# Kernel optimization log

Hardware: AMD Instinct MI355X
Metric: run time of the kernel (lower is better)

## Reference

```python
import jax, jax.numpy as jnp
import numpy as np

DELTA = 1
DROP_DC = False
EPS = 1e-8


def _shell_labels(D, H, W, delta):
    # radial frequency magnitude in cycles/voxel, assuming cubic-ish volume
    fx = jnp.fft.fftfreq(D)[:, None, None]
    fy = jnp.fft.fftfreq(H)[None, :, None]
    fz = jnp.fft.fftfreq(W)[None, None, :]
    r = jnp.sqrt(fx * fx + fy * fy + fz * fz)  # [D,H,W]
    n = min(D, H, W)
    nbins = n // (2 * delta)          # shells up to Nyquist (0.5 cyc/voxel)
    df = delta / n                    # shell width in frequency units
    labels = jnp.minimum((r / df).astype(jnp.int32), nbins)  # overflow bin = nbins
    return labels.reshape(-1), nbins


def setup_inputs() -> dict:
    key = jax.random.key(0)
    k1, k2 = jax.random.split(key)
    shape = (2, 1, 256, 256, 256)
    img_ref = jax.random.normal(k1, shape, dtype=jnp.float32)
    img_pred = jax.random.normal(k2, shape, dtype=jnp.float32)
    return {"img_ref": img_ref, "img_pred": img_pred}


def reference(img_ref, img_pred):
    B, C, D, H, W = img_ref.shape
    labels, nbins = _shell_labels(D, H, W, DELTA)

    F1 = jnp.fft.fftn(img_ref, axes=(-3, -2, -1))   # complex64 [B,C,D,H,W]
    F2 = jnp.fft.fftn(img_pred, axes=(-3, -2, -1))

    cross = jnp.real(F1 * jnp.conj(F2)).reshape(B * C, -1)
    p1 = (jnp.real(F1) ** 2 + jnp.imag(F1) ** 2).reshape(B * C, -1)
    p2 = (jnp.real(F2) ** 2 + jnp.imag(F2) ** 2).reshape(B * C, -1)

    def seg(x):  # radial shell sum; drop the overflow bin beyond Nyquist
        return jax.ops.segment_sum(x, labels, num_segments=nbins + 1)[:nbins]

    num = jax.vmap(seg)(cross)   # [B*C, nbins]
    d1 = jax.vmap(seg)(p1)
    d2 = jax.vmap(seg)(p2)

    fsc = num / jnp.sqrt(d1 * d2 + EPS)
    if DROP_DC:
        fsc = fsc[:, 1:]
    loss = 1.0 - jnp.mean(fsc ** 2)
    return loss
```

## Files before the change

kernel.cpp:

```cpp
#include <hip/hip_runtime.h>
#include <math.h>

#define NDIM 256
#define VOL  (NDIM*NDIM*NDIM)
#define NB   128

__device__ __forceinline__ int dr4(int x) {
    int b = (int)(__brev((unsigned)x) >> 24);
    return ((b >> 1) & 0x55) | ((b << 1) & 0xAA);
}
__device__ __forceinline__ float2 cmul(float2 a, float2 b) {
    return make_float2(a.x * b.x - a.y * b.y, a.x * b.y + a.y * b.x);
}
__device__ __forceinline__ float2 cadd(float2 a, float2 b){ return make_float2(a.x+b.x, a.y+b.y); }
__device__ __forceinline__ float2 csub(float2 a, float2 b){ return make_float2(a.x-b.x, a.y-b.y); }
__device__ __forceinline__ float2 cmuli_neg(float2 a){ return make_float2(a.y, -a.x); }
__device__ __forceinline__ float2 cmuli_pos(float2 a){ return make_float2(-a.y, a.x); }

__global__ __launch_bounds__(256) void fftz_pack(const float* __restrict__ re_in,
                                                 const float* __restrict__ im_in,
                                                 float2* __restrict__ out)
{
    __shared__ float2 buf[4][2][NDIM];
    const int t = threadIdx.x;
    const int w = t >> 6, j = t & 63;
    const int L = blockIdx.x * 4 + w;
    const float* rp = re_in + (size_t)L * NDIM;
    const float* ip = im_in + (size_t)L * NDIM;

    float2 v0 = make_float2(rp[j      ], ip[j      ]);
    float2 v1 = make_float2(rp[j +  64], ip[j +  64]);
    float2 v2 = make_float2(rp[j + 128], ip[j + 128]);
    float2 v3 = make_float2(rp[j + 192], ip[j + 192]);

    {
        float2 t0=cadd(v0,v2), t1=csub(v0,v2), t2=cadd(v1,v3), t3=csub(v1,v3);
        buf[w][0][4*j    ] = cadd(t0, t2);
        buf[w][0][4*j + 1] = cadd(t1, cmuli_neg(t3));
        buf[w][0][4*j + 2] = csub(t0, t2);
        buf[w][0][4*j + 3] = cadd(t1, cmuli_pos(t3));
    }
    __builtin_amdgcn_sched_barrier(0);

    int p = 0;
    #pragma unroll
    for (int stage = 1; stage <= 2; ++stage) {
        const int Ns = (stage == 1) ? 4 : 16;
        const int jm = j & (Ns - 1);
        float2 a0 = buf[w][p][j      ];
        float2 a1 = buf[w][p][j +  64];
        float2 a2 = buf[w][p][j + 128];
        float2 a3 = buf[w][p][j + 192];
        float sn, cs;
        __sincosf(-(float)(2.0 * M_PI) * (float)jm / (float)(4 * Ns), &sn, &cs);
        float2 w1 = make_float2(cs, sn);
        float2 w2 = cmul(w1, w1);
        float2 w3 = cmul(w2, w1);
        a1 = cmul(a1, w1); a2 = cmul(a2, w2); a3 = cmul(a3, w3);
        float2 t0=cadd(a0,a2), t1=csub(a0,a2), t2=cadd(a1,a3), t3=csub(a1,a3);
        const int idxD = (j / Ns) * (4 * Ns) + jm;
        buf[w][p^1][idxD         ] = cadd(t0, t2);
        buf[w][p^1][idxD +     Ns] = cadd(t1, cmuli_neg(t3));
        buf[w][p^1][idxD + 2 * Ns] = csub(t0, t2);
        buf[w][p^1][idxD + 3 * Ns] = cadd(t1, cmuli_pos(t3));
        p ^= 1;
        __builtin_amdgcn_sched_barrier(0);
    }

    {
        float2 a0 = buf[w][p][j      ];
        float2 a1 = buf[w][p][j +  64];
        float2 a2 = buf[w][p][j + 128];
        float2 a3 = buf[w][p][j + 192];
        float sn, cs;
        __sincosf(-(float)(2.0 * M_PI) * (float)j / 256.0f, &sn, &cs);
        float2 w1 = make_float2(cs, sn);
        float2 w2 = cmul(w1, w1);
        float2 w3 = cmul(w2, w1);
        a1 = cmul(a1, w1); a2 = cmul(a2, w2); a3 = cmul(a3, w3);
        float2 t0=cadd(a0,a2), t1=csub(a0,a2), t2=cadd(a1,a3), t3=csub(a1,a3);
        float2* op = out + (size_t)L * NDIM;
        op[j      ] = cadd(t0, t2);
        op[j +  64] = cadd(t1, cmuli_neg(t3));
        op[j + 128] = csub(t0, t2);
        op[j + 192] = cadd(t1, cmuli_pos(t3));
    }
}

__global__ __launch_bounds__(256) void fft_strided(float2* __restrict__ A,
                                                   int lineStride, int outerStride)
{
    __shared__ __align__(16) float2 tile[NDIM * 18];
    __shared__ float2 tw[NDIM];
    const int t = threadIdx.x;
    {
        float sn, cs;
        __sincosf(-(float)(2.0 * M_PI) * (float)t / 256.0f, &sn, &cs);
        tw[t] = make_float2(cs, sn);
    }
    const int l4 = t & 7, u8 = t >> 3;
    const int o = blockIdx.x >> 4, c = blockIdx.x & 15;
    const long long base = (long long)o * outerStride + c * 16;

    #pragma unroll
    for (int it = 0; it < 8; ++it) {
        int pos = u8 + it * 32;
        const float4 d = *(const float4*)&A[base + (long long)pos * lineStride + 2 * l4];
        tile[pos * 18 + 2 * l4    ] = make_float2(d.x, d.y);
        tile[pos * 18 + 2 * l4 + 1] = make_float2(d.z, d.w);
    }
    __syncthreads();

    const int l = t & 15, u = t >> 4;
    #pragma unroll
    for (int ls = 6; ls >= 0; ls -= 2) {
        const int s = 1 << ls;
        #pragma unroll
        for (int it = 0; it < 4; ++it) {
            int m  = u + it * 16;
            int jm = m & (s - 1);
            int bidx = ((m >> ls) << (ls + 2)) + jm;
            float2 a  = tile[(bidx        ) * 18 + l];
            float2 b  = tile[(bidx +     s) * 18 + l];
            float2 cc = tile[(bidx + 2 * s) * 18 + l];
            float2 d  = tile[(bidx + 3 * s) * 18 + l];
            float2 t0=cadd(a,cc), t1=csub(a,cc), t2=cadd(b,d), t3=csub(b,d);
            float2 y0 = cadd(t0, t2);
            float2 y1 = cadd(t1, cmuli_neg(t3));
            float2 y2 = csub(t0, t2);
            float2 y3 = cadd(t1, cmuli_pos(t3));
            int k1 = jm << (6 - ls);
            y1 = cmul(y1, tw[k1]);
            y2 = cmul(y2, tw[2 * k1]);
            y3 = cmul(y3, tw[3 * k1]);
            tile[(bidx        ) * 18 + l] = y0;
            tile[(bidx +     s) * 18 + l] = y1;
            tile[(bidx + 2 * s) * 18 + l] = y2;
            tile[(bidx + 3 * s) * 18 + l] = y3;
        }
        __syncthreads();
    }

    #pragma unroll
    for (int it = 0; it < 8; ++it) {
        int pos = u8 + it * 32;
        float2 e0 = tile[pos * 18 + 2 * l4], e1 = tile[pos * 18 + 2 * l4 + 1];
        *(float4*)&A[base + (long long)pos * lineStride + 2 * l4] =
            make_float4(e0.x, e0.y, e1.x, e1.y);
    }
}

__global__ __launch_bounds__(256) void reduce_shells(const float2* __restrict__ A,
                                                     float* __restrict__ bins)
{
    __shared__ __align__(16) float2 lines[8][2][NDIM];
    __shared__ float bs[4][3 * NB];
    const int t = threadIdx.x;
    const int w = t >> 6;
    for (int i = t; i < 4 * 3 * NB; i += 256) ((float*)bs)[i] = 0.f;

    int  Lk[8], Lpk[8], lc2[8];
    float wgt[8];
    #pragma unroll
    for (int jj = 0; jj < 8; ++jj) {
        int L = blockIdx.x * 8 + jj;
        int px = L >> 8, py = L & 255;
        int fx = dr4(px), fy = dr4(py);
        int fxp = (256 - fx) & 255, fyp = (256 - fy) & 255;
        int Lp = dr4(fxp) * 256 + dr4(fyp);
        int ax = (fx < 128) ? fx : 256 - fx;
        int ay = (fy < 128) ? fy : 256 - fy;
        int c2 = ax * ax + ay * ay;
        lc2[jj] = -1;
        if (Lp >= L && c2 < NB * NB) lc2[jj] = c2;
        Lk[jj]  = (lc2[jj] < 0) ? 0 : L;
        Lpk[jj] = (lc2[jj] < 0) ? 0 : Lp;
        wgt[jj] = (Lp == L) ? 1.f : 2.f;
    }

    const int sel  = t >> 7;
    const int idx4 = t & 127;
    #pragma unroll
    for (int jj = 0; jj < 8; ++jj) {
        int line = sel ? Lpk[jj] : Lk[jj];
        const float4 d = *(const float4*)&A[(size_t)line * 256 + 2 * idx4];
        *(float4*)&lines[jj][sel][2 * idx4] = d;
    }
    __syncthreads();

    const int pz  = t;
    const int izc = (pz < 128) ? pz : 256 - pz;
    const int iz2 = izc * izc;
    const int pzp = (256 - pz) & 255;

    #pragma unroll
    for (int jj = 0; jj < 8; ++jj) {
        if (lc2[jj] < 0) continue;
        int m = lc2[jj] + iz2;
        int lab = (int)sqrtf((float)m);
        if (lab >= NB) continue;
        float2 a = lines[jj][0][pz];
        float2 b = lines[jj][1][pzp];
        float F1r = 0.5f * (a.x + b.x);
        float F1i = 0.5f * (a.y - b.y);
        float F2r = 0.5f * (a.y + b.y);
        float F2i = 0.5f * (b.x - a.x);
        float g = wgt[jj];
        atomicAdd(&bs[w][lab],           g * (F1r * F2r + F1i * F2i));
        atomicAdd(&bs[w][NB + lab],      g * (F1r * F1r + F1i * F1i));
        atomicAdd(&bs[w][2 * NB + lab],  g * (F2r * F2r + F2i * F2i));
    }
    __syncthreads();

    for (int i = t; i < 3 * NB; i += 256) {
        float v = bs[0][i] + bs[1][i] + bs[2][i] + bs[3][i];
        if (v != 0.f) atomicAdd(&bins[i], v);
    }
}

__global__ void zero_bins(float* bins)
{
    int t = blockIdx.x * blockDim.x + threadIdx.x;
    if (t < 2 * 3 * NB) bins[t] = 0.f;
}

__global__ void finalize(const float* __restrict__ binsAll, float* __restrict__ out)
{
    __shared__ float red[256];
    const int t = threadIdx.x;
    const int b = t >> 7, bin = t & 127;
    const float* bb = binsAll + b * 3 * NB;
    float num = bb[bin], d1 = bb[NB + bin], d2 = bb[2 * NB + bin];
    float fsc = num / sqrtf(d1 * d2 + 1e-8f);
    red[t] = fsc * fsc;
    __syncthreads();
    for (int s = 128; s > 0; s >>= 1) {
        if (t < s) red[t] += red[t + s];
        __syncthreads();
    }
    if (t == 0) out[0] = 1.f - red[0] / 256.f;
}

__global__ void ws_too_small(float* out) { out[0] = -1.0e9f; }

extern "C" void kernel_launch(void* const* d_in, const int* in_sizes, int n_in,
                              void* d_out, int out_size, void* d_ws, size_t ws_size,
                              hipStream_t stream)
{
    const float* ref  = (const float*)d_in[0];
    const float* pred = (const float*)d_in[1];
    float* out = (float*)d_out;

    const size_t volBytes = (size_t)VOL * sizeof(float2);
    if (ws_size < volBytes + 4096) {
        ws_too_small<<<1, 1, 0, stream>>>(out);
        return;
    }
    float2* A   = (float2*)d_ws;
    float* bins = (float*)((char*)d_ws + volBytes);

    zero_bins<<<1, 1024, 0, stream>>>(bins);

    for (int b = 0; b < 2; ++b) {
        fftz_pack  <<<16384, 256, 0, stream>>>(ref + (size_t)b * VOL,
                                               pred + (size_t)b * VOL, A);
        fft_strided<<<4096, 256, 0, stream>>>(A, 256,   65536);
        fft_strided<<<4096, 256, 0, stream>>>(A, 65536, 256);
        reduce_shells<<<8192, 256, 0, stream>>>(A, bins + b * 3 * NB);
    }
    finalize<<<1, 256, 0, stream>>>(bins, out);
}
```

Before: 671.2 us.

## Restructure shell reduction so each warp handles one line with run-length bin accumulation

The shell reduction now gives each 32-thread group one (x,y) line, and each thread walks 8 consecutive z positions. Per-bin contributions are accumulated in registers and flushed to the shared-memory histogram only when the shell label changes, which cuts LDS atomics sharply. The line staging buffer is padded to avoid bank conflicts, and the histogram copies drop from four to two. Inactive lines now idle whole warps instead of single iterations, which may cost some load balance.

```diff
diff --git a/kernel.cpp b/kernel.cpp
--- a/kernel.cpp
+++ b/kernel.cpp
@@ -4,6 +4,7 @@
 #define NDIM 256
 #define VOL  (NDIM*NDIM*NDIM)
 #define NB   128
+#define LDIM 272
 
 __device__ __forceinline__ int dr4(int x) {
     int b = (int)(__brev((unsigned)x) >> 24);
@@ -153,14 +154,12 @@
 __global__ __launch_bounds__(256) void reduce_shells(const float2* __restrict__ A,
                                                      float* __restrict__ bins)
 {
-    __shared__ __align__(16) float2 lines[8][2][NDIM];
-    __shared__ float bs[4][3 * NB];
-    const int t = threadIdx.x;
-    const int w = t >> 6;
-    for (int i = t; i < 4 * 3 * NB; i += 256) ((float*)bs)[i] = 0.f;
-
-    int  Lk[8], Lpk[8], lc2[8];
-    float wgt[8];
+    __shared__ __align__(16) float2 lines[8][2][LDIM];
+    __shared__ float bs[2][3 * NB];
+    const int t = threadIdx.x;
+    for (int i = t; i < 2 * 3 * NB; i += 256) ((float*)bs)[i] = 0.f;
+
+    int Lk[8], Lpk[8];
     #pragma unroll
     for (int jj = 0; jj < 8; ++jj) {
         int L = blockIdx.x * 8 + jj;
@@ -171,11 +170,9 @@
         int ax = (fx < 128) ? fx : 256 - fx;
         int ay = (fy < 128) ? fy : 256 - fy;
         int c2 = ax * ax + ay * ay;
-        lc2[jj] = -1;
-        if (Lp >= L && c2 < NB * NB) lc2[jj] = c2;
-        Lk[jj]  = (lc2[jj] < 0) ? 0 : L;
-        Lpk[jj] = (lc2[jj] < 0) ? 0 : Lp;
-        wgt[jj] = (Lp == L) ? 1.f : 2.f;
+        bool act = (Lp >= L) && (c2 < NB * NB);
+        Lk[jj]  = act ? L  : 0;
+        Lpk[jj] = act ? Lp : 0;
     }
 
     const int sel  = t >> 7;
@@ -184,36 +181,64 @@
     for (int jj = 0; jj < 8; ++jj) {
         int line = sel ? Lpk[jj] : Lk[jj];
         const float4 d = *(const float4*)&A[(size_t)line * 256 + 2 * idx4];
-        *(float4*)&lines[jj][sel][2 * idx4] = d;
-    }
-    __syncthreads();
-
-    const int pz  = t;
-    const int izc = (pz < 128) ? pz : 256 - pz;
-    const int iz2 = izc * izc;
-    const int pzp = (256 - pz) & 255;
-
-    #pragma unroll
-    for (int jj = 0; jj < 8; ++jj) {
-        if (lc2[jj] < 0) continue;
-        int m = lc2[jj] + iz2;
-        int lab = (int)sqrtf((float)m);
-        if (lab >= NB) continue;
-        float2 a = lines[jj][0][pz];
-        float2 b = lines[jj][1][pzp];
-        float F1r = 0.5f * (a.x + b.x);
-        float F1i = 0.5f * (a.y - b.y);
-        float F2r = 0.5f * (a.y + b.y);
-        float F2i = 0.5f * (b.x - a.x);
-        float g = wgt[jj];
-        atomicAdd(&bs[w][lab],           g * (F1r * F2r + F1i * F2i));
-        atomicAdd(&bs[w][NB + lab],      g * (F1r * F1r + F1i * F1i));
-        atomicAdd(&bs[w][2 * NB + lab],  g * (F2r * F2r + F2i * F2i));
+        int z = 2 * idx4;
+        *(float4*)&lines[jj][sel][z + (z >> 4)] = d;
+    }
+    __syncthreads();
+
+    const int jj = t >> 5;
+    const int l  = t & 31;
+    {
+        int L = blockIdx.x * 8 + jj;
+        int px = L >> 8, py = L & 255;
+        int fx = dr4(px), fy = dr4(py);
+        int fxp = (256 - fx) & 255, fyp = (256 - fy) & 255;
+        int Lp = dr4(fxp) * 256 + dr4(fyp);
+        int ax = (fx < 128) ? fx : 256 - fx;
+        int ay = (fy < 128) ? fy : 256 - fy;
+        int c2 = ax * ax + ay * ay;
+        if (Lp >= L && c2 < NB * NB) {
+            const float g = (Lp == L) ? 1.f : 2.f;
+            const int w2 = t >> 7;
+            int curLab = -1;
+            float a0 = 0.f, a1 = 0.f, a2 = 0.f;
+            #pragma unroll
+            for (int k = 0; k < 8; ++k) {
+                const int pz  = l * 8 + k;
+                const int izc = (pz < 128) ? pz : 256 - pz;
+                const int lab = (int)sqrtf((float)(c2 + izc * izc));
+                const int zp  = (256 - pz) & 255;
+                float2 a = lines[jj][0][pz + (pz >> 4)];
+                float2 b = lines[jj][1][zp + (zp >> 4)];
+                float F1r = 0.5f * (a.x + b.x);
+                float F1i = 0.5f * (a.y - b.y);
+                float F2r = 0.5f * (a.y + b.y);
+                float F2i = 0.5f * (b.x - a.x);
+                float v0 = g * (F1r * F2r + F1i * F2i);
+                float v1 = g * (F1r * F1r + F1i * F1i);
+                float v2 = g * (F2r * F2r + F2i * F2i);
+                if (lab != curLab) {
+                    if (curLab >= 0 && curLab < NB) {
+                        atomicAdd(&bs[w2][curLab],          a0);
+                        atomicAdd(&bs[w2][NB + curLab],     a1);
+                        atomicAdd(&bs[w2][2 * NB + curLab], a2);
+                    }
+                    curLab = lab; a0 = v0; a1 = v1; a2 = v2;
+                } else {
+                    a0 += v0; a1 += v1; a2 += v2;
+                }
+            }
+            if (curLab >= 0 && curLab < NB) {
+                atomicAdd(&bs[w2][curLab],          a0);
+                atomicAdd(&bs[w2][NB + curLab],     a1);
+                atomicAdd(&bs[w2][2 * NB + curLab], a2);
+            }
+        }
     }
     __syncthreads();
 
     for (int i = t; i < 3 * NB; i += 256) {
-        float v = bs[0][i] + bs[1][i] + bs[2][i] + bs[3][i];
+        float v = bs[0][i] + bs[1][i];
         if (v != 0.f) atomicAdd(&bins[i], v);
     }
 }
```

Measured after the change: 653.7 us. -2.6%, faster.
